# Kernel tuning notes

Measured on AMD Instinct MI355X. Metric: run time of the kernel, lower is better.

The kernel has to match this reference:

```python
import jax, jax.numpy as jnp
import numpy as np

N, D_IN, D_OUT, E = 8192, 2048, 8192, 8


def setup_inputs() -> dict:
    key = jax.random.key(0)
    k1, k2, k3 = jax.random.split(key, 3)
    x = jax.random.normal(k1, (N, D_IN), dtype=jnp.float32)
    # packed weight layout [E, in, out] (pack() pretransposes [E,out,in] -> [E,in,out])
    weight = jax.random.normal(k2, (E, D_IN, D_OUT), dtype=jnp.float32) * (1.0 / np.sqrt(D_IN))
    indices = jax.random.randint(k3, (N,), 0, E, dtype=jnp.int32)
    return {"x": x, "weight": weight, "indices": indices}


def reference(x, weight, indices):
    # gather_mm: out[n] = x[n] @ weight[indices[n]]  -> [N, D_OUT]
    # Avoid materializing weight[indices] ([N, in, out]); instead loop over the
    # small fixed expert count, masking tokens routed to each expert.
    n_experts = weight.shape[0]
    out = jnp.zeros((x.shape[0], weight.shape[-1]), dtype=x.dtype)
    for e in range(n_experts):
        mask = (indices == e)[:, None]
        xe = jnp.where(mask, x, 0)          # zero out tokens not routed to e
        out = out + xe @ weight[e]           # [N, in] @ [in, out]
    return out
```

## Files before the change

kernel.cpp:

```cpp
#include <hip/hip_runtime.h>
#include <hip/hip_bf16.h>
#include <stdint.h>

#define N_TOK 8192
#define D_IN  2048
#define D_OUT 8192
#define NEXP  8
#define NT_MAX 72
#define KSTEPS 32
#define NSTRIPS 64
#define IMG_B  16384
#define X_OFF  65536
#define X_BYTES (NT_MAX * KSTEPS * IMG_B)
#define W_OFF  (X_OFF + X_BYTES)
#define W_BYTES ((long)NEXP * NSTRIPS * KSTEPS * IMG_B)
#define WS_NEED ((size_t)W_OFF + (size_t)W_BYTES)


typedef float  f32x4  __attribute__((ext_vector_type(4)));
typedef __bf16 bf16x8 __attribute__((ext_vector_type(8)));

__global__ void SwitchLinear_setup_kernel(const int* __restrict__ idx,
                                          int* __restrict__ ws) {
    __shared__ int cnt[NEXP], cur[NEXP];
    int t = threadIdx.x;
    if (t < NEXP) cnt[t] = 0;
    __syncthreads();
    for (int i = t; i < N_TOK; i += 256) atomicAdd(&cnt[idx[i]], 1);
    __syncthreads();
    if (t == 0) {
        int o = 0, nt = 0;
        for (int e = 0; e < NEXP; ++e) {
            cur[e] = o;
            int c = cnt[e];
            for (int r = 0; r < c; r += 128) {
                ws[8 + nt]   = e;
                ws[96 + nt]  = o + r;
                ws[192 + nt] = (c - r < 128) ? (c - r) : 128;
                ++nt;
            }
            o += c;
        }
        ws[0] = nt;
    }
    __syncthreads();
    for (int i = t; i < N_TOK; i += 256) {
        int p = atomicAdd(&cur[idx[i]], 1);
        ws[512 + p] = i;
    }
}



__global__ __launch_bounds__(256) void SwitchLinear_convx_kernel(
    const float* __restrict__ x, const int* __restrict__ ws,
    char* __restrict__ wsb) {
    const int tile = blockIdx.x, kst = blockIdx.y;
    if (tile >= ws[0]) return;
    const int rs = ws[96 + tile], rows = ws[192 + tile];
    char* img = wsb + X_OFF + (long)(tile * KSTEPS + kst) * IMG_B;
    const int t = threadIdx.x;
#pragma unroll
    for (int i = 0; i < 4; ++i) {
        int u = t + i * 256;
        int r = u >> 3, kc = u & 7;
        int rl = rs + (r < rows ? r : rows - 1);
        int token = ws[512 + rl];
        const float* src = x + (long)token * D_IN + kst * 64 + kc * 8;
        f32x4 v0 = *(const f32x4*)src;
        f32x4 v1 = *(const f32x4*)(src + 4);
        union { __bf16 h[8]; uint4 u4; } c;
        c.h[0] = (__bf16)v0[0]; c.h[1] = (__bf16)v0[1];
        c.h[2] = (__bf16)v0[2]; c.h[3] = (__bf16)v0[3];
        c.h[4] = (__bf16)v1[0]; c.h[5] = (__bf16)v1[1];
        c.h[6] = (__bf16)v1[2]; c.h[7] = (__bf16)v1[3];
        *(uint4*)(img + r * 128 + ((kc ^ (r & 7)) << 4)) = c.u4;
    }
}

__global__ __launch_bounds__(256) void SwitchLinear_convw_kernel(
    const float* __restrict__ w, char* __restrict__ wsb) {
    const int img = blockIdx.x;
    const int kst = img & 31, strip = (img >> 5) & 63, e = img >> 11;
    __shared__ float tl[64 * 129];
    const float* src = w + (long)e * D_IN * D_OUT + (long)(kst * 64) * D_OUT + strip * 128;
    const int t = threadIdx.x;
#pragma unroll
    for (int i = 0; i < 8; ++i) {
        int u = t + i * 256;
        int row = u >> 5, ch = u & 31;
        f32x4 v = *(const f32x4*)(src + (long)row * D_OUT + ch * 4);
        float* d = &tl[row * 129 + ch * 4];
        d[0] = v[0]; d[1] = v[1]; d[2] = v[2]; d[3] = v[3];
    }
    __syncthreads();
    char* dimg = wsb + W_OFF + (long)img * IMG_B;
#pragma unroll
    for (int i = 0; i < 4; ++i) {
        int u = t + i * 256;
        int n = u >> 3, kc = u & 7;
        union { __bf16 h[8]; uint4 u4; } c;
#pragma unroll
        for (int j = 0; j < 8; ++j) c.h[j] = (__bf16)tl[(kc * 8 + j) * 129 + n];
        *(uint4*)(dimg + n * 128 + ((kc ^ (n & 7)) << 4)) = c.u4;
    }
}

__global__ __launch_bounds__(256, 3) void SwitchLinear_gemm_kernel(
    const char* __restrict__ wsb, const int* __restrict__ ws,
    float* __restrict__ out) {
    const int bid = blockIdx.x;
    const int lb  = (bid & 7) * (NT_MAX * NSTRIPS / 8) + (bid >> 3);
    const int tx  = lb % NT_MAX;
    const int y   = lb / NT_MAX;
    if (tx >= ws[0]) return;
    const int e = ws[8 + tx], rs = ws[96 + tx], rows = ws[192 + tx];

    __shared__ __align__(16) unsigned short As[128 * 64];
    __shared__ __align__(16) unsigned short Bs[128 * 64];
    __shared__ int ord[128];

    const int t = threadIdx.x;
    if (t < 128) {
        int r = (t < rows) ? (rs + t) : rs;
        ord[t] = ws[512 + r];
    }

    const char* aBase = wsb + X_OFF + (long)(tx * KSTEPS) * IMG_B;
    const char* bBase = wsb + W_OFF + (long)((e * NSTRIPS + y) * KSTEPS) * IMG_B;

    const int lane = t & 63;
    const int wid  = t >> 6;
    const int wr = wid >> 1, wc = wid & 1;
    const int lm = lane & 15, lk = lane >> 4;

    f32x4 acc[4][4];
#pragma unroll
    for (int i = 0; i < 4; ++i)
#pragma unroll
        for (int j = 0; j < 4; ++j) acc[i][j] = (f32x4){0.f, 0.f, 0.f, 0.f};

    for (int kt = 0; kt < KSTEPS; ++kt) {
        const char* aImg = aBase + kt * IMG_B;
        const char* bImg = bBase + kt * IMG_B;
#pragma unroll
        for (int i = 0; i < 4; ++i) {
            const int off = i * 4096 + t * 16;
            __builtin_amdgcn_global_load_lds(
                (const __attribute__((address_space(1))) uint32_t*)(aImg + off),
                (__attribute__((address_space(3))) uint32_t*)((char*)As + off),
                16, 0, 0);
            __builtin_amdgcn_global_load_lds(
                (const __attribute__((address_space(1))) uint32_t*)(bImg + off),
                (__attribute__((address_space(3))) uint32_t*)((char*)Bs + off),
                16, 0, 0);
        }
        __syncthreads();
#pragma unroll
        for (int ks = 0; ks < 2; ++ks) {
            const int cbase = ks * 4 + lk;
            bf16x8 a[4], b[4];
#pragma unroll
            for (int mi = 0; mi < 4; ++mi) {
                int r = wr * 64 + mi * 16 + lm;
                a[mi] = *(const bf16x8*)((const char*)As + r * 128 + ((cbase ^ (r & 7)) << 4));
            }
#pragma unroll
            for (int ni = 0; ni < 4; ++ni) {
                int n = wc * 64 + ni * 16 + lm;
                b[ni] = *(const bf16x8*)((const char*)Bs + n * 128 + ((cbase ^ (n & 7)) << 4));
            }
#pragma unroll
            for (int mi = 0; mi < 4; ++mi)
#pragma unroll
                for (int ni = 0; ni < 4; ++ni)
                    acc[mi][ni] = __builtin_amdgcn_mfma_f32_16x16x32_bf16(
                        a[mi], b[ni], acc[mi][ni], 0, 0, 0);
        }
        __syncthreads();
    }

#pragma unroll
    for (int mi = 0; mi < 4; ++mi) {
#pragma unroll
        for (int j = 0; j < 4; ++j) {
            int rl = wr * 64 + mi * 16 + lk * 4 + j;
            if (rl < rows) {
                int token = ord[rl];
                float* po = out + (long)token * D_OUT + y * 128 + wc * 64 + lm;
#pragma unroll
                for (int ni = 0; ni < 4; ++ni) po[ni * 16] = acc[mi][ni][j];
            }
        }
    }
}


__device__ __forceinline__ int fb_a_byte(int r, int kbyte) {
    return r * 128 + (kbyte ^ ((r & 7) << 4));
}
__device__ __forceinline__ int fb_b_byte(int n, int kbyte) {
    int slot = (n ^ (n >> 2)) & 7;
    return n * 128 + (kbyte ^ (slot << 4));
}

__global__ __launch_bounds__(256, 2) void SwitchLinear_gemm_fb_kernel(
    const float* __restrict__ x, const float* __restrict__ w,
    const int* __restrict__ ws, float* __restrict__ out) {
    const int nt = ws[0];
    const int tx = blockIdx.x;
    if (tx >= nt) return;
    const int e    = ws[8 + tx];
    const int rs   = ws[96 + tx];
    const int rows = ws[192 + tx];
    const int col0 = blockIdx.y * 128;

    __shared__ __align__(16) unsigned short As[128 * 64];
    __shared__ __align__(16) unsigned short Bs[128 * 64];
    __shared__ int ord[128];

    const int t = threadIdx.x;
    if (t < 128) {
        int r = (t < rows) ? (rs + t) : rs;
        ord[t] = ws[512 + r];
    }
    __syncthreads();

    const int kq = t & 15;
    const float* pA[8];
    int rowA[8];
#pragma unroll
    for (int i = 0; i < 8; ++i) {
        int r = (t >> 4) + 16 * i;
        rowA[i] = r;
        pA[i] = x + (long)ord[r] * D_IN + kq * 4;
    }
    const float* pB[2];
    int nB[2], kbB[2];
#pragma unroll
    for (int i = 0; i < 2; ++i) {
        int u = t + 256 * i;
        int kg = u >> 5, q = u & 31;
        kbB[i] = kg * 4;
        nB[i]  = q * 4;
        pB[i]  = w + (long)e * D_IN * D_OUT + (long)(kg * 4) * D_OUT + col0 + q * 4;
    }

    const int lane = t & 63;
    const int wid  = t >> 6;
    const int wr = wid >> 1, wc = wid & 1;
    const int lm = lane & 15, lk = lane >> 4;

    f32x4 acc[4][4];
#pragma unroll
    for (int i = 0; i < 4; ++i)
#pragma unroll
        for (int j = 0; j < 4; ++j) acc[i][j] = (f32x4){0.f, 0.f, 0.f, 0.f};

    for (int k0 = 0; k0 < D_IN; k0 += 64) {
#pragma unroll
        for (int i = 0; i < 8; ++i) {
            f32x4 v = *(const f32x4*)(pA[i] + k0);
            union { __bf16 h[4]; uint2 u; } c;
            c.h[0] = (__bf16)v[0]; c.h[1] = (__bf16)v[1];
            c.h[2] = (__bf16)v[2]; c.h[3] = (__bf16)v[3];
            *(uint2*)((char*)As + fb_a_byte(rowA[i], kq * 8)) = c.u;
        }
#pragma unroll
        for (int i = 0; i < 2; ++i) {
            const float* p = pB[i] + (long)k0 * D_OUT;
            f32x4 r0 = *(const f32x4*)(p);
            f32x4 r1 = *(const f32x4*)(p + D_OUT);
            f32x4 r2 = *(const f32x4*)(p + 2 * D_OUT);
            f32x4 r3 = *(const f32x4*)(p + 3 * D_OUT);
#pragma unroll
            for (int j = 0; j < 4; ++j) {
                int n = nB[i] + j;
                union { __bf16 h[4]; uint2 u; } c;
                c.h[0] = (__bf16)r0[j]; c.h[1] = (__bf16)r1[j];
                c.h[2] = (__bf16)r2[j]; c.h[3] = (__bf16)r3[j];
                *(uint2*)((char*)Bs + fb_b_byte(n, kbB[i] * 2)) = c.u;
            }
        }
        __syncthreads();
#pragma unroll
        for (int ks = 0; ks < 2; ++ks) {
            bf16x8 a[4], b[4];
            const int kbyte = ks * 64 + lk * 16;
#pragma unroll
            for (int mi = 0; mi < 4; ++mi) {
                int r = wr * 64 + mi * 16 + lm;
                a[mi] = *(const bf16x8*)((const char*)As + fb_a_byte(r, kbyte));
            }
#pragma unroll
            for (int ni = 0; ni < 4; ++ni) {
                int n = wc * 64 + ni * 16 + lm;
                b[ni] = *(const bf16x8*)((const char*)Bs + fb_b_byte(n, kbyte));
            }
#pragma unroll
            for (int mi = 0; mi < 4; ++mi)
#pragma unroll
                for (int ni = 0; ni < 4; ++ni)
                    acc[mi][ni] = __builtin_amdgcn_mfma_f32_16x16x32_bf16(
                        a[mi], b[ni], acc[mi][ni], 0, 0, 0);
        }
        __syncthreads();
    }
#pragma unroll
    for (int mi = 0; mi < 4; ++mi) {
#pragma unroll
        for (int j = 0; j < 4; ++j) {
            int rl = wr * 64 + mi * 16 + lk * 4 + j;
            if (rl < rows) {
                int token = ord[rl];
                float* po = out + (long)token * D_OUT + col0 + wc * 64 + lm;
#pragma unroll
                for (int ni = 0; ni < 4; ++ni) po[ni * 16] = acc[mi][ni][j];
            }
        }
    }
}

extern "C" void kernel_launch(void* const* d_in, const int* in_sizes, int n_in,
                              void* d_out, int out_size, void* d_ws, size_t ws_size,
                              hipStream_t stream) {
    const float* x   = (const float*)d_in[0];
    const float* w   = (const float*)d_in[1];
    const int*   idx = (const int*)d_in[2];
    float* out = (float*)d_out;
    int*   ws  = (int*)d_ws;
    char*  wsb = (char*)d_ws;

    SwitchLinear_setup_kernel<<<1, 256, 0, stream>>>(idx, ws);
    if (ws_size >= WS_NEED) {
        SwitchLinear_convx_kernel<<<dim3(NT_MAX, KSTEPS), 256, 0, stream>>>(x, ws, wsb);
        SwitchLinear_convw_kernel<<<NEXP * NSTRIPS * KSTEPS, 256, 0, stream>>>(w, wsb);
        SwitchLinear_gemm_kernel<<<NT_MAX * NSTRIPS, 256, 0, stream>>>(wsb, ws, out);
    } else {
        dim3 grid(NT_MAX, NSTRIPS);
        SwitchLinear_gemm_fb_kernel<<<grid, 256, 0, stream>>>(x, w, ws, out);
    }
}
```

Baseline: 616.5 us.

## Enlarge GEMM tiles to 256x256 with double-buffered LDS pipeline and 8 waves

Switches the main GEMM to 256x256 output tiles computed by 512 threads. Loads are double-buffered through LDS, with prefetch of the next k-step interleaved between MFMA phases and prioritised using setprio and barriers. The staged bf16 images for x and weights are relaid into 64-byte-row half images with a new swizzle to match. Setup keeps a separate 128-row tile list for the fallback path. Larger tiles cut global and LDS traffic per FLOP, but each CU runs a single block and padded rows waste more work.

```diff
diff --git a/kernel.cpp b/kernel.cpp
--- a/kernel.cpp
+++ b/kernel.cpp
@@ -6,15 +6,15 @@
 #define D_IN  2048
 #define D_OUT 8192
 #define NEXP  8
-#define NT_MAX 72
-#define KSTEPS 32
-#define NSTRIPS 64
-#define IMG_B  16384
-#define X_OFF  65536
-#define X_BYTES (NT_MAX * KSTEPS * IMG_B)
-#define W_OFF  (X_OFF + X_BYTES)
-#define W_BYTES ((long)NEXP * NSTRIPS * KSTEPS * IMG_B)
-#define WS_NEED ((size_t)W_OFF + (size_t)W_BYTES)
+#define KST   32
+#define NT2   40
+#define NS2   32
+#define AIMG  32768
+#define X_OFF2 65536
+#define X_BYTES2 ((long)NT2 * KST * AIMG)
+#define W_OFF2 (X_OFF2 + X_BYTES2)
+#define W_BYTES2 ((long)NEXP * NS2 * KST * AIMG)
+#define WS_NEED2 ((size_t)(W_OFF2 + W_BYTES2))
 
 
 typedef float  f32x4  __attribute__((ext_vector_type(4)));
@@ -29,19 +29,26 @@
     for (int i = t; i < N_TOK; i += 256) atomicAdd(&cnt[idx[i]], 1);
     __syncthreads();
     if (t == 0) {
-        int o = 0, nt = 0;
+        int o = 0, nt = 0, nt1 = 0;
         for (int e = 0; e < NEXP; ++e) {
             cur[e] = o;
             int c = cnt[e];
-            for (int r = 0; r < c; r += 128) {
+            for (int r = 0; r < c; r += 256) {
                 ws[8 + nt]   = e;
                 ws[96 + nt]  = o + r;
-                ws[192 + nt] = (c - r < 128) ? (c - r) : 128;
+                ws[192 + nt] = (c - r < 256) ? (c - r) : 256;
                 ++nt;
             }
+            for (int r = 0; r < c; r += 128) {
+                ws[256 + nt1] = e;
+                ws[328 + nt1] = o + r;
+                ws[400 + nt1] = (c - r < 128) ? (c - r) : 128;
+                ++nt1;
+            }
             o += c;
         }
         ws[0] = nt;
+        ws[4] = nt1;
     }
     __syncthreads();
     for (int i = t; i < N_TOK; i += 256) {
@@ -49,7 +56,6 @@
         ws[512 + p] = i;
     }
 }
-
 
 
 __global__ __launch_bounds__(256) void SwitchLinear_convx_kernel(
@@ -58,32 +64,37 @@
     const int tile = blockIdx.x, kst = blockIdx.y;
     if (tile >= ws[0]) return;
     const int rs = ws[96 + tile], rows = ws[192 + tile];
-    char* img = wsb + X_OFF + (long)(tile * KSTEPS + kst) * IMG_B;
+    char* img = wsb + X_OFF2 + (long)(tile * KST + kst) * AIMG;
     const int t = threadIdx.x;
 #pragma unroll
-    for (int i = 0; i < 4; ++i) {
+    for (int i = 0; i < 8; ++i) {
         int u = t + i * 256;
-        int r = u >> 3, kc = u & 7;
-        int rl = rs + (r < rows ? r : rows - 1);
+        int h = u >> 10, rem = u & 1023;
+        int r = rem >> 3, kc8 = rem & 7;
+        int R = h * 128 + r;
+        int rl = rs + (R < rows ? R : rows - 1);
         int token = ws[512 + rl];
-        const float* src = x + (long)token * D_IN + kst * 64 + kc * 8;
+        const float* src = x + (long)token * D_IN + kst * 64 + kc8 * 8;
         f32x4 v0 = *(const f32x4*)src;
         f32x4 v1 = *(const f32x4*)(src + 4);
-        union { __bf16 h[8]; uint4 u4; } c;
-        c.h[0] = (__bf16)v0[0]; c.h[1] = (__bf16)v0[1];
-        c.h[2] = (__bf16)v0[2]; c.h[3] = (__bf16)v0[3];
-        c.h[4] = (__bf16)v1[0]; c.h[5] = (__bf16)v1[1];
-        c.h[6] = (__bf16)v1[2]; c.h[7] = (__bf16)v1[3];
-        *(uint4*)(img + r * 128 + ((kc ^ (r & 7)) << 4)) = c.u4;
+        union { __bf16 hh[8]; uint4 u4; } c;
+        c.hh[0] = (__bf16)v0[0]; c.hh[1] = (__bf16)v0[1];
+        c.hh[2] = (__bf16)v0[2]; c.hh[3] = (__bf16)v0[3];
+        c.hh[4] = (__bf16)v1[0]; c.hh[5] = (__bf16)v1[1];
+        c.hh[6] = (__bf16)v1[2]; c.hh[7] = (__bf16)v1[3];
+        *(uint4*)(img + h * 16384 + (kc8 >> 2) * 8192 + r * 64 +
+                  (((kc8 & 3) ^ (r & 3)) << 4)) = c.u4;
     }
 }
 
 __global__ __launch_bounds__(256) void SwitchLinear_convw_kernel(
     const float* __restrict__ w, char* __restrict__ wsb) {
     const int img = blockIdx.x;
-    const int kst = img & 31, strip = (img >> 5) & 63, e = img >> 11;
+    const int kst = img & 31, s = (img >> 5) & 63, e = img >> 11;
+    const int y = s >> 1, h = s & 1;
     __shared__ float tl[64 * 129];
-    const float* src = w + (long)e * D_IN * D_OUT + (long)(kst * 64) * D_OUT + strip * 128;
+    const float* src = w + (long)e * D_IN * D_OUT + (long)(kst * 64) * D_OUT +
+                       y * 256 + h * 128;
     const int t = threadIdx.x;
 #pragma unroll
     for (int i = 0; i < 8; ++i) {
@@ -94,105 +105,144 @@
         d[0] = v[0]; d[1] = v[1]; d[2] = v[2]; d[3] = v[3];
     }
     __syncthreads();
-    char* dimg = wsb + W_OFF + (long)img * IMG_B;
+    char* dimg = wsb + W_OFF2 + (long)((e * NS2 + y) * KST + kst) * AIMG + h * 16384;
 #pragma unroll
     for (int i = 0; i < 4; ++i) {
         int u = t + i * 256;
-        int n = u >> 3, kc = u & 7;
-        union { __bf16 h[8]; uint4 u4; } c;
-#pragma unroll
-        for (int j = 0; j < 8; ++j) c.h[j] = (__bf16)tl[(kc * 8 + j) * 129 + n];
-        *(uint4*)(dimg + n * 128 + ((kc ^ (n & 7)) << 4)) = c.u4;
-    }
-}
-
-__global__ __launch_bounds__(256, 3) void SwitchLinear_gemm_kernel(
+        int cc = u >> 3, kc8 = u & 7;
+        union { __bf16 hh[8]; uint4 u4; } c;
+#pragma unroll
+        for (int j = 0; j < 8; ++j) c.hh[j] = (__bf16)tl[(kc8 * 8 + j) * 129 + cc];
+        *(uint4*)(dimg + (kc8 >> 2) * 8192 + cc * 64 +
+                  (((kc8 & 3) ^ (cc & 3)) << 4)) = c.u4;
+    }
+}
+
+
+__global__ __launch_bounds__(512, 1) void SwitchLinear_gemm_kernel(
     const char* __restrict__ wsb, const int* __restrict__ ws,
     float* __restrict__ out) {
     const int bid = blockIdx.x;
-    const int lb  = (bid & 7) * (NT_MAX * NSTRIPS / 8) + (bid >> 3);
-    const int tx  = lb % NT_MAX;
-    const int y   = lb / NT_MAX;
+    const int lb  = (bid & 7) * ((NT2 * NS2) / 8) + (bid >> 3);
+    const int tx  = lb % NT2;
+    const int y   = lb / NT2;
     if (tx >= ws[0]) return;
     const int e = ws[8 + tx], rs = ws[96 + tx], rows = ws[192 + tx];
 
-    __shared__ __align__(16) unsigned short As[128 * 64];
-    __shared__ __align__(16) unsigned short Bs[128 * 64];
-    __shared__ int ord[128];
+    __shared__ __align__(16) char lds[2][2][2][2][8192];
+    __shared__ int ord[256];
 
     const int t = threadIdx.x;
-    if (t < 128) {
-        int r = (t < rows) ? (rs + t) : rs;
-        ord[t] = ws[512 + r];
-    }
-
-    const char* aBase = wsb + X_OFF + (long)(tx * KSTEPS) * IMG_B;
-    const char* bBase = wsb + W_OFF + (long)((e * NSTRIPS + y) * KSTEPS) * IMG_B;
+    if (t < 256) ord[t] = ws[512 + rs + (t < rows ? t : 0)];
+    __syncthreads();
+
+    const char* aImg = wsb + X_OFF2 + (long)(tx * KST) * AIMG;
+    const char* bImg = wsb + W_OFF2 + (long)((e * NS2 + y) * KST) * AIMG;
 
     const int lane = t & 63;
     const int wid  = t >> 6;
-    const int wr = wid >> 1, wc = wid & 1;
+    const int wr = wid >> 2, wc = wid & 3;
     const int lm = lane & 15, lk = lane >> 4;
 
-    f32x4 acc[4][4];
-#pragma unroll
-    for (int i = 0; i < 4; ++i)
+    f32x4 acc[8][4];
+#pragma unroll
+    for (int i = 0; i < 8; ++i)
 #pragma unroll
         for (int j = 0; j < 4; ++j) acc[i][j] = (f32x4){0.f, 0.f, 0.f, 0.f};
 
-    for (int kt = 0; kt < KSTEPS; ++kt) {
-        const char* aImg = aBase + kt * IMG_B;
-        const char* bImg = bBase + kt * IMG_B;
-#pragma unroll
-        for (int i = 0; i < 4; ++i) {
-            const int off = i * 4096 + t * 16;
-            __builtin_amdgcn_global_load_lds(
-                (const __attribute__((address_space(1))) uint32_t*)(aImg + off),
-                (__attribute__((address_space(3))) uint32_t*)((char*)As + off),
-                16, 0, 0);
-            __builtin_amdgcn_global_load_lds(
-                (const __attribute__((address_space(1))) uint32_t*)(bImg + off),
-                (__attribute__((address_space(3))) uint32_t*)((char*)Bs + off),
-                16, 0, 0);
-        }
-        __syncthreads();
-#pragma unroll
-        for (int ks = 0; ks < 2; ++ks) {
-            const int cbase = ks * 4 + lk;
-            bf16x8 a[4], b[4];
-#pragma unroll
-            for (int mi = 0; mi < 4; ++mi) {
-                int r = wr * 64 + mi * 16 + lm;
-                a[mi] = *(const bf16x8*)((const char*)As + r * 128 + ((cbase ^ (r & 7)) << 4));
-            }
-#pragma unroll
-            for (int ni = 0; ni < 4; ++ni) {
-                int n = wc * 64 + ni * 16 + lm;
-                b[ni] = *(const bf16x8*)((const char*)Bs + n * 128 + ((cbase ^ (n & 7)) << 4));
-            }
-#pragma unroll
-            for (int mi = 0; mi < 4; ++mi)
-#pragma unroll
-                for (int ni = 0; ni < 4; ++ni)
-                    acc[mi][ni] = __builtin_amdgcn_mfma_f32_16x16x32_bf16(
-                        a[mi], b[ni], acc[mi][ni], 0, 0, 0);
-        }
-        __syncthreads();
-    }
-
-#pragma unroll
-    for (int mi = 0; mi < 4; ++mi) {
+    bf16x8 aa[4], bb[4];
+
+#define STG(op, h, ks, tt)                                                    \
+    __builtin_amdgcn_global_load_lds(                                         \
+        (const __attribute__((address_space(1))) uint32_t*)(                  \
+            ((op) ? bImg : aImg) + (long)(tt) * AIMG + (h) * 16384 +          \
+            (ks) * 8192 + t * 16),                                            \
+        (__attribute__((address_space(3))) uint32_t*)(                        \
+            &lds[(tt) & 1][op][h][ks][t * 16]),                               \
+        16, 0, 0)
+
+#define LDB(p, ks)                                                            \
+    do { _Pragma("unroll")                                                    \
+        for (int ni = 0; ni < 4; ++ni) {                                      \
+            int cc = (wc & 1) * 64 + ni * 16 + lm;                            \
+            bb[ni] = *(const bf16x8*)(&lds[p][1][wc >> 1][ks]                 \
+                         [cc * 64 + ((lk ^ (cc & 3)) << 4)]);                 \
+        } } while (0)
+
+#define LDA(p, ks, mh)                                                        \
+    do { _Pragma("unroll")                                                    \
+        for (int q = 0; q < 4; ++q) {                                         \
+            int rr = (mh) * 64 + q * 16 + lm;                                 \
+            aa[q] = *(const bf16x8*)(&lds[p][0][wr][ks]                       \
+                         [rr * 64 + ((lk ^ (rr & 3)) << 4)]);                 \
+        } } while (0)
+
+#define MFMA16(mh)                                                            \
+    do { _Pragma("unroll")                                                    \
+        for (int q = 0; q < 4; ++q)                                           \
+            _Pragma("unroll")                                                 \
+            for (int ni = 0; ni < 4; ++ni)                                    \
+                acc[(mh) * 4 + q][ni] = __builtin_amdgcn_mfma_f32_16x16x32_bf16( \
+                    aa[q], bb[ni], acc[(mh) * 4 + q][ni], 0, 0, 0);           \
+    } while (0)
+
+#define PH(p, ks, mh, DOB, ISSUE, WAITASM)                                    \
+    do {                                                                      \
+        if (DOB) LDB(p, ks);                                                  \
+        LDA(p, ks, mh);                                                       \
+        ISSUE;                                                                \
+        WAITASM;                                                              \
+        __builtin_amdgcn_s_barrier();                                         \
+        asm volatile("s_waitcnt lgkmcnt(0)" ::: "memory");                    \
+        __builtin_amdgcn_sched_barrier(0);                                    \
+        __builtin_amdgcn_s_setprio(1);                                        \
+        MFMA16(mh);                                                           \
+        __builtin_amdgcn_s_setprio(0);                                        \
+        __builtin_amdgcn_s_barrier();                                         \
+    } while (0)
+
+    STG(0, 0, 0, 0); STG(0, 1, 0, 0); STG(1, 0, 0, 0); STG(1, 1, 0, 0);
+    STG(0, 0, 1, 0); STG(0, 1, 1, 0); STG(1, 0, 1, 0); STG(1, 1, 1, 0);
+    asm volatile("s_waitcnt vmcnt(4)" ::: "memory");
+    __builtin_amdgcn_s_barrier();
+
+    for (int tt = 0; tt < KST - 1; ++tt) {
+        const int p = tt & 1;
+        const int nx = tt + 1;
+        PH(p, 0, 0, 1, { STG(0, 0, 0, nx); STG(0, 1, 0, nx); }, ((void)0));
+        PH(p, 0, 1, 0, { STG(1, 0, 0, nx); STG(1, 1, 0, nx); },
+           asm volatile("s_waitcnt vmcnt(4)" ::: "memory"));
+        PH(p, 1, 0, 1, { STG(0, 0, 1, nx); STG(0, 1, 1, nx); }, ((void)0));
+        PH(p, 1, 1, 0, { STG(1, 0, 1, nx); STG(1, 1, 1, nx); },
+           asm volatile("s_waitcnt vmcnt(4)" ::: "memory"));
+    }
+    {
+        const int p = (KST - 1) & 1;
+        PH(p, 0, 0, 1, ((void)0), ((void)0));
+        PH(p, 0, 1, 0, ((void)0),
+           asm volatile("s_waitcnt vmcnt(0)" ::: "memory"));
+        PH(p, 1, 0, 1, ((void)0), ((void)0));
+        PH(p, 1, 1, 0, ((void)0), ((void)0));
+    }
+
+#pragma unroll
+    for (int mi = 0; mi < 8; ++mi) {
 #pragma unroll
         for (int j = 0; j < 4; ++j) {
-            int rl = wr * 64 + mi * 16 + lk * 4 + j;
+            int rl = wr * 128 + mi * 16 + lk * 4 + j;
             if (rl < rows) {
                 int token = ord[rl];
-                float* po = out + (long)token * D_OUT + y * 128 + wc * 64 + lm;
+                float* po = out + (long)token * D_OUT + y * 256 + wc * 64 + lm;
 #pragma unroll
                 for (int ni = 0; ni < 4; ++ni) po[ni * 16] = acc[mi][ni][j];
             }
         }
     }
+#undef STG
+#undef LDB
+#undef LDA
+#undef MFMA16
+#undef PH
 }
 
 
@@ -207,12 +257,12 @@
 __global__ __launch_bounds__(256, 2) void SwitchLinear_gemm_fb_kernel(
     const float* __restrict__ x, const float* __restrict__ w,
     const int* __restrict__ ws, float* __restrict__ out) {
-    const int nt = ws[0];
+    const int nt = ws[4];
     const int tx = blockIdx.x;
     if (tx >= nt) return;
-    const int e    = ws[8 + tx];
-    const int rs   = ws[96 + tx];
-    const int rows = ws[192 + tx];
+    const int e    = ws[256 + tx];
+    const int rs   = ws[328 + tx];
+    const int rows = ws[400 + tx];
     const int col0 = blockIdx.y * 128;
 
     __shared__ __align__(16) unsigned short As[128 * 64];
@@ -332,12 +382,12 @@
     char*  wsb = (char*)d_ws;
 
     SwitchLinear_setup_kernel<<<1, 256, 0, stream>>>(idx, ws);
-    if (ws_size >= WS_NEED) {
-        SwitchLinear_convx_kernel<<<dim3(NT_MAX, KSTEPS), 256, 0, stream>>>(x, ws, wsb);
-        SwitchLinear_convw_kernel<<<NEXP * NSTRIPS * KSTEPS, 256, 0, stream>>>(w, wsb);
-        SwitchLinear_gemm_kernel<<<NT_MAX * NSTRIPS, 256, 0, stream>>>(wsb, ws, out);
+    if (ws_size >= WS_NEED2) {
+        SwitchLinear_convx_kernel<<<dim3(NT2, KST), 256, 0, stream>>>(x, ws, wsb);
+        SwitchLinear_convw_kernel<<<NEXP * 64 * KST, 256, 0, stream>>>(w, wsb);
+        SwitchLinear_gemm_kernel<<<NT2 * NS2, 512, 0, stream>>>(wsb, ws, out);
     } else {
-        dim3 grid(NT_MAX, NSTRIPS);
+        dim3 grid(72, 64);
         SwitchLinear_gemm_fb_kernel<<<grid, 256, 0, stream>>>(x, w, ws, out);
     }
 }
```

Result: faster. 597.8 us (-3.0%).
